# Optimization experiments

Measured on AMD Instinct MI355X. Metric: run time of the kernel, lower is better.

The kernel has to match this reference:

```python
import jax, jax.numpy as jnp
import numpy as np

CUTOFF = 5.0
B, A, N, G, F = 32, 256, 64, 50, 128


def _ssp(v):
    # shifted softplus used by SchNet filter network
    return jax.nn.softplus(v) - jnp.log(2.0).astype(v.dtype)


def setup_inputs() -> dict:
    key = jax.random.key(0)
    ks = jax.random.split(key, 8)
    x = jax.random.normal(ks[0], (B, A, F), dtype=jnp.float32)
    r_ij = jax.random.uniform(ks[1], (B, A, N), dtype=jnp.float32) * 4.5
    f_ij = jax.random.normal(ks[2], (B, A, N, G), dtype=jnp.float32)
    pairwise_mask = jnp.ones((B, A, N), dtype=jnp.float32)
    neighbors = jax.random.randint(ks[3], (B, A, N), 0, A, dtype=jnp.int64)
    in2f_w = jax.random.normal(ks[4], (F, F), dtype=jnp.float32) / np.sqrt(F)
    fw1 = jax.random.normal(ks[5], (G, F), dtype=jnp.float32) / np.sqrt(G)
    fb1 = jnp.zeros((F,), dtype=jnp.float32)
    fw2 = jax.random.normal(ks[6], (F, F), dtype=jnp.float32) / np.sqrt(F)
    fb2 = jnp.zeros((F,), dtype=jnp.float32)
    return {"x": x, "r_ij": r_ij, "f_ij": f_ij, "pairwise_mask": pairwise_mask,
            "neighbors": neighbors, "in2f_w": in2f_w, "fw1": fw1, "fb1": fb1,
            "fw2": fw2, "fb2": fb2}


def reference(x, r_ij, f_ij, pairwise_mask, neighbors, in2f_w, fw1, fb1, fw2, fb2):
    # filter network: Dense(G->F, shifted softplus) -> Dense(F->F, linear)
    W = _ssp(jnp.einsum('bang,gf->banf', f_ij, fw1) + fb1)
    W = jnp.einsum('banh,hf->banf', W, fw2) + fb2          # (B,A,N,F)
    # cosine cutoff
    C = 0.5 * (jnp.cos(r_ij * (jnp.pi / CUTOFF)) + 1.0)
    C = C * (r_ij < CUTOFF).astype(r_ij.dtype)
    W = W * C[..., None]
    # in2f dense (no bias)
    y = jnp.einsum('bai,if->baf', x, in2f_w)               # (B,A,F)
    # gather neighbor features along atom axis
    b_idx = jnp.arange(B)[:, None, None]
    y_nbh = y[b_idx, neighbors]                             # (B,A,N,F)
    # elementwise filter multiply + masked sum over neighbor axis
    out = jnp.sum(y_nbh * W * pairwise_mask[..., None], axis=2)  # (B,A,F)
    return out
```

## Files before the change

kernel.cpp:

```cpp
#include <hip/hip_runtime.h>
#include <hip/hip_bf16.h>
#include <math.h>

#define Bdim 32
#define Adim 256
#define Ndim 64
#define Gdim 50
#define Fdim 128

typedef __attribute__((ext_vector_type(8)))  short short8;
typedef __attribute__((ext_vector_type(16))) float floatx16;

__device__ __forceinline__ unsigned short f2bf_u(float x) {
    __hip_bfloat16 h = __float2bfloat16(x);
    return __builtin_bit_cast(unsigned short, h);
}
__device__ __forceinline__ unsigned pk2bf(float a, float b) {
    return (unsigned)f2bf_u(a) | ((unsigned)f2bf_u(b) << 16);
}
__device__ __forceinline__ float bf2f(unsigned short v) {
    return __builtin_bit_cast(float, ((unsigned)v) << 16);
}
__device__ __forceinline__ float sspf(float v) {
    float t = __expf(-fabsf(v));
    return fmaxf(v, 0.0f) + __logf(1.0f + t) - 0.69314718056f;
}
__device__ __forceinline__ short8 mk8(unsigned a, unsigned b, unsigned c, unsigned d) {
    union { unsigned u[4]; short8 s; } t;
    t.u[0] = a; t.u[1] = b; t.u[2] = c; t.u[3] = d;
    return t.s;
}

__global__ __launch_bounds__(256) void in2f_mfma2(const float* __restrict__ x,
                                                  const float* __restrict__ w,
                                                  unsigned short* __restrict__ y) {
    __shared__ short sWT[128 * 132];
    __shared__ short sX [128 * 132];
    const int tid = threadIdx.x;

#pragma unroll 4
    for (int k = 0; k < 32; ++k) {
        int idx = tid + k * 256;
        float2 v = *(const float2*)(w + 2 * idx);
        int i = idx >> 6;
        int f = (2 * idx) & 127;
        sWT[f * 132 + i]       = (short)f2bf_u(v.x);
        sWT[(f + 1) * 132 + i] = (short)f2bf_u(v.y);
    }
    const float* xb = x + (size_t)blockIdx.x * (128 * 128);
#pragma unroll 4
    for (int k = 0; k < 32; ++k) {
        int idx = tid + k * 256;
        float2 v = *(const float2*)(xb + 2 * idx);
        int row = idx >> 6;
        int i = (2 * idx) & 127;
        *(unsigned*)&sX[row * 132 + i] = pk2bf(v.x, v.y);
    }
    __syncthreads();

    const int wv = tid >> 6, lane = tid & 63, lm = lane & 31, lh = lane >> 5;
    floatx16 acc[4];
#pragma unroll
    for (int jt = 0; jt < 4; ++jt)
#pragma unroll
        for (int e = 0; e < 16; ++e) acc[jt][e] = 0.0f;

#pragma unroll
    for (int ks = 0; ks < 8; ++ks) {
        int g0 = ks * 16 + lh * 8;
        const short* ap = &sX[(wv * 32 + lm) * 132 + g0];
        uint2 a0 = *(const uint2*)ap;
        uint2 a1 = *(const uint2*)(ap + 4);
        short8 a = mk8(a0.x, a0.y, a1.x, a1.y);
#pragma unroll
        for (int jt = 0; jt < 4; ++jt) {
            const short* bp = &sWT[(jt * 32 + lm) * 132 + g0];
            uint2 b0 = *(const uint2*)bp;
            uint2 b1 = *(const uint2*)(bp + 4);
            acc[jt] = __builtin_amdgcn_mfma_f32_32x32x16_bf16(
                a, mk8(b0.x, b0.y, b1.x, b1.y), acc[jt], 0, 0, 0);
        }
    }
    const int rbase = blockIdx.x * 128 + wv * 32;
#pragma unroll
    for (int jt = 0; jt < 4; ++jt)
#pragma unroll
        for (int r = 0; r < 16; ++r) {
            int row = rbase + (r & 3) + 8 * (r >> 2) + 4 * lh;
            y[(size_t)row * 128 + jt * 32 + lm] = f2bf_u(acc[jt][r]);
        }
}

#define SF1 68
#define SF2 132
#define SFI 60

__global__ __launch_bounds__(256, 2) void cfconv_mfma3(
    const float* __restrict__ r_ij, const float* __restrict__ f_ij,
    const float* __restrict__ mask, const int* __restrict__ nbr,
    const float* __restrict__ fw1, const float* __restrict__ fb1,
    const float* __restrict__ fw2, const float* __restrict__ fb2,
    const unsigned short* __restrict__ ybf, float* __restrict__ out)
{
    __shared__ short sFw1[128 * SF1];
    __shared__ short sFw2[128 * SF2];
    __shared__ short sFij[128 * SFI + 16];
    __shared__ float sCm[128];
    __shared__ int   sNbr[128];
    __shared__ float sRed[4 * 128];

    const int tid = threadIdx.x, wv = tid >> 6, lane = tid & 63;
    const int lm = lane & 31, lh = lane >> 5;

    for (int idx = tid; idx < Gdim * 128; idx += 256) {
        int g = idx >> 7, f = idx & 127;
        sFw1[f * SF1 + g] = (short)f2bf_u(fw1[idx]);
    }
    for (int idx = tid; idx < 128 * 14; idx += 256) {
        int f = idx / 14, g = Gdim + idx % 14;
        sFw1[f * SF1 + g] = (g == Gdim) ? (short)f2bf_u(fb1[f]) : (short)0;
    }
    for (int idx = tid; idx < 128 * 128; idx += 256) {
        int h = idx >> 7, f = idx & 127;
        sFw2[f * SF2 + h] = (short)f2bf_u(fw2[idx]);
    }
    for (int idx = tid; idx < 128 * 5; idx += 256) {
        int row = idx / 5, k = idx - row * 5;
        *(unsigned*)&sFij[row * SFI + 50 + 2 * k] = (k == 0) ? 0x00003F80u : 0u;
    }
    if (tid < 8) *(unsigned*)&sFij[128 * SFI + 2 * tid] = 0u;

    float fb2v[4];
#pragma unroll
    for (int jt = 0; jt < 4; ++jt) fb2v[jt] = fb2[jt * 32 + lm];

    for (int it = 0; it < 4; ++it) {
        const int sp = blockIdx.x + 1024 * it;

        const float* fp = f_ij + (size_t)sp * (2 * Ndim * Gdim);
#pragma unroll
        for (int k = 0; k < 13; ++k) {
            int idx = tid + k * 256;
            if (idx < 3200) {
                float2 v = *(const float2*)(fp + 2 * idx);
                int row = idx / 25;
                int g   = 2 * idx - row * 50;
                *(unsigned*)&sFij[row * SFI + g] = pk2bf(v.x, v.y);
            }
        }
        if (tid < 128) {
            int site = sp * 2 + (tid >> 6), n = tid & 63;
            float r = r_ij[(size_t)site * Ndim + n];
            float c = 0.5f * (__cosf(r * 0.62831853071796f) + 1.0f);
            c = (r < 5.0f) ? c : 0.0f;
            sCm[tid]  = c * mask[(size_t)site * Ndim + n];
            sNbr[tid] = nbr[(size_t)site * Ndim + n];
        }
        __syncthreads();

        const int rowb = wv * 32;
        unsigned A2[8][4];
#pragma unroll
        for (int ft = 0; ft < 4; ++ft) {
            floatx16 a1;
#pragma unroll
            for (int e = 0; e < 16; ++e) a1[e] = 0.0f;
#pragma unroll
            for (int ks = 0; ks < 4; ++ks) {
                int g0 = ks * 16 + lh * 8;
                const short* ap = &sFw1[(ft * 32 + lm) * SF1 + g0];
                uint2 a0 = *(const uint2*)ap;
                uint2 a1v = *(const uint2*)(ap + 4);
                const short* bp = &sFij[(rowb + lm) * SFI + g0];
                uint2 b0 = *(const uint2*)bp;
                uint2 b1v = *(const uint2*)(bp + 4);
                a1 = __builtin_amdgcn_mfma_f32_32x32x16_bf16(
                    mk8(a0.x, a0.y, a1v.x, a1v.y),
                    mk8(b0.x, b0.y, b1v.x, b1v.y), a1, 0, 0, 0);
            }
            unsigned P[8], X[8];
#pragma unroll
            for (int q = 0; q < 8; ++q)
                P[q] = pk2bf(sspf(a1[2 * q]), sspf(a1[2 * q + 1]));
#pragma unroll
            for (int q = 0; q < 8; ++q) X[q] = (unsigned)__shfl_xor((int)P[q], 32);
            A2[2*ft][0]   = lh ? X[2] : P[0];  A2[2*ft][1]   = lh ? X[3] : P[1];
            A2[2*ft][2]   = lh ? P[2] : X[0];  A2[2*ft][3]   = lh ? P[3] : X[1];
            A2[2*ft+1][0] = lh ? X[6] : P[4];  A2[2*ft+1][1] = lh ? X[7] : P[5];
            A2[2*ft+1][2] = lh ? P[6] : X[4];  A2[2*ft+1][3] = lh ? P[7] : X[5];
        }

        floatx16 acc2[4];
#pragma unroll
        for (int jt = 0; jt < 4; ++jt)
#pragma unroll
            for (int e = 0; e < 16; ++e) acc2[jt][e] = 0.0f;
#pragma unroll
        for (int ks = 0; ks < 8; ++ks) {
            short8 a = mk8(A2[ks][0], A2[ks][1], A2[ks][2], A2[ks][3]);
#pragma unroll
            for (int jt = 0; jt < 4; ++jt) {
                const short* bp = &sFw2[(jt * 32 + lm) * SF2 + ks * 16 + lh * 8];
                uint2 b0 = *(const uint2*)bp;
                uint2 b1 = *(const uint2*)(bp + 4);
                acc2[jt] = __builtin_amdgcn_mfma_f32_32x32x16_bf16(
                    a, mk8(b0.x, b0.y, b1.x, b1.y), acc2[jt], 0, 0, 0);
            }
        }

        const int ps = sp * 2 + (wv >> 1);
        float cmv[16]; int nbv[16];
#pragma unroll
        for (int rq = 0; rq < 4; ++rq) {
            float4 c4 = *(const float4*)&sCm[wv * 32 + rq * 8 + lh * 4];
            int4   n4 = *(const int4*)&sNbr[wv * 32 + rq * 8 + lh * 4];
            cmv[rq*4+0] = c4.x; cmv[rq*4+1] = c4.y; cmv[rq*4+2] = c4.z; cmv[rq*4+3] = c4.w;
            nbv[rq*4+0] = n4.x; nbv[rq*4+1] = n4.y; nbv[rq*4+2] = n4.z; nbv[rq*4+3] = n4.w;
        }
        const int bofs = (ps >> 8) * Adim;
        float part[4] = {0.f, 0.f, 0.f, 0.f};
#pragma unroll
        for (int r = 0; r < 16; ++r) {
            float cm = cmv[r];
            const unsigned short* yr = ybf + (size_t)(bofs + nbv[r]) * 128;
#pragma unroll
            for (int jt = 0; jt < 4; ++jt) {
                float yv = bf2f(yr[jt * 32 + lm]);
                part[jt] += (acc2[jt][r] + fb2v[jt]) * cm * yv;
            }
        }
#pragma unroll
        for (int jt = 0; jt < 4; ++jt) {
            float s = part[jt] + __shfl_xor(part[jt], 32);
            if (lh == 0) sRed[wv * 128 + jt * 32 + lm] = s;
        }
        __syncthreads();
        {
            int s = tid >> 7, f = tid & 127;
            out[(size_t)(sp * 2 + s) * 128 + f] =
                sRed[(2 * s) * 128 + f] + sRed[(2 * s + 1) * 128 + f];
        }
    }
}

extern "C" void kernel_launch(void* const* d_in, const int* in_sizes, int n_in,
                              void* d_out, int out_size, void* d_ws, size_t ws_size,
                              hipStream_t stream) {
    const float* x      = (const float*)d_in[0];
    const float* r_ij   = (const float*)d_in[1];
    const float* f_ij   = (const float*)d_in[2];
    const float* mask   = (const float*)d_in[3];
    const int*   nbr    = (const int*)d_in[4];
    const float* in2f_w = (const float*)d_in[5];
    const float* fw1    = (const float*)d_in[6];
    const float* fb1    = (const float*)d_in[7];
    const float* fw2    = (const float*)d_in[8];
    const float* fb2    = (const float*)d_in[9];
    float* out = (float*)d_out;
    unsigned short* y = (unsigned short*)d_ws;

    in2f_mfma2<<<64, 256, 0, stream>>>(x, in2f_w, y);
    cfconv_mfma3<<<1024, 256, 0, stream>>>(r_ij, f_ij, mask, nbr,
                                           fw1, fb1, fw2, fb2, y, out);
}
```

Baseline: 253.6 us.

## Move fw1 prep to separate kernel, cut LDS, raise occupancy, cheaper bf16/ssp math

Adds a small prep kernel that writes a transposed bf16 fw1 (with the bias folded in) to workspace, so the main kernel reads it straight from global/L2 and no longer keeps it in shared memory. The freed LDS lets launch bounds go from 2 to 3 blocks per CU. It also swaps the library bf16 conversion for a manual round-to-nearest-even, simplifies the shifted softplus to exp2/log2, hoists the f_ij fragment loads out of the filter loop, and splits in2f over 256 blocks that read x directly from global. Risks: the simplified softplus can overflow for large inputs, the manual rounding does not handle NaN, the extra launch adds overhead, and the higher occupancy target may cause register spills.

```diff
diff --git a/kernel.cpp b/kernel.cpp
--- a/kernel.cpp
+++ b/kernel.cpp
@@ -1,5 +1,4 @@
 #include <hip/hip_runtime.h>
-#include <hip/hip_bf16.h>
 #include <math.h>
 
 #define Bdim 32
@@ -11,19 +10,22 @@
 typedef __attribute__((ext_vector_type(8)))  short short8;
 typedef __attribute__((ext_vector_type(16))) float floatx16;
 
+__device__ __forceinline__ unsigned bfround(float x) {
+    unsigned u = __builtin_bit_cast(unsigned, x);
+    return u + 0x7FFFu + ((u >> 16) & 1u);
+}
 __device__ __forceinline__ unsigned short f2bf_u(float x) {
-    __hip_bfloat16 h = __float2bfloat16(x);
-    return __builtin_bit_cast(unsigned short, h);
+    return (unsigned short)(bfround(x) >> 16);
 }
 __device__ __forceinline__ unsigned pk2bf(float a, float b) {
-    return (unsigned)f2bf_u(a) | ((unsigned)f2bf_u(b) << 16);
+    return (bfround(a) >> 16) | (bfround(b) & 0xFFFF0000u);
 }
 __device__ __forceinline__ float bf2f(unsigned short v) {
     return __builtin_bit_cast(float, ((unsigned)v) << 16);
 }
 __device__ __forceinline__ float sspf(float v) {
-    float t = __expf(-fabsf(v));
-    return fmaxf(v, 0.0f) + __logf(1.0f + t) - 0.69314718056f;
+    float t = __builtin_exp2f(v * 1.44269504089f);
+    return fmaf(__builtin_log2f(1.0f + t), 0.69314718056f, -0.69314718056f);
 }
 __device__ __forceinline__ short8 mk8(unsigned a, unsigned b, unsigned c, unsigned d) {
     union { unsigned u[4]; short8 s; } t;
@@ -31,13 +33,20 @@
     return t.s;
 }
 
-__global__ __launch_bounds__(256) void in2f_mfma2(const float* __restrict__ x,
-                                                  const float* __restrict__ w,
-                                                  unsigned short* __restrict__ y) {
+__global__ __launch_bounds__(256) void prep_fw1t(const float* __restrict__ fw1,
+                                                 const float* __restrict__ fb1,
+                                                 unsigned short* __restrict__ fw1t) {
+    int idx = blockIdx.x * 256 + threadIdx.x;
+    int f = idx >> 6, g = idx & 63;
+    float v = (g < Gdim) ? fw1[g * Fdim + f] : ((g == Gdim) ? fb1[f] : 0.0f);
+    fw1t[idx] = f2bf_u(v);
+}
+
+__global__ __launch_bounds__(256) void in2f_v3(const float* __restrict__ x,
+                                               const float* __restrict__ w,
+                                               unsigned short* __restrict__ y) {
     __shared__ short sWT[128 * 132];
-    __shared__ short sX [128 * 132];
     const int tid = threadIdx.x;
-
 #pragma unroll 4
     for (int k = 0; k < 32; ++k) {
         int idx = tid + k * 256;
@@ -47,62 +56,45 @@
         sWT[f * 132 + i]       = (short)f2bf_u(v.x);
         sWT[(f + 1) * 132 + i] = (short)f2bf_u(v.y);
     }
-    const float* xb = x + (size_t)blockIdx.x * (128 * 128);
-#pragma unroll 4
-    for (int k = 0; k < 32; ++k) {
-        int idx = tid + k * 256;
-        float2 v = *(const float2*)(xb + 2 * idx);
-        int row = idx >> 6;
-        int i = (2 * idx) & 127;
-        *(unsigned*)&sX[row * 132 + i] = pk2bf(v.x, v.y);
-    }
     __syncthreads();
 
     const int wv = tid >> 6, lane = tid & 63, lm = lane & 31, lh = lane >> 5;
-    floatx16 acc[4];
-#pragma unroll
-    for (int jt = 0; jt < 4; ++jt)
-#pragma unroll
-        for (int e = 0; e < 16; ++e) acc[jt][e] = 0.0f;
-
+    const int rbase = blockIdx.x * 32;
+    floatx16 acc;
+#pragma unroll
+    for (int e = 0; e < 16; ++e) acc[e] = 0.0f;
+
+    const float* xr = x + (size_t)(rbase + lm) * Fdim;
 #pragma unroll
     for (int ks = 0; ks < 8; ++ks) {
         int g0 = ks * 16 + lh * 8;
-        const short* ap = &sX[(wv * 32 + lm) * 132 + g0];
-        uint2 a0 = *(const uint2*)ap;
-        uint2 a1 = *(const uint2*)(ap + 4);
-        short8 a = mk8(a0.x, a0.y, a1.x, a1.y);
-#pragma unroll
-        for (int jt = 0; jt < 4; ++jt) {
-            const short* bp = &sWT[(jt * 32 + lm) * 132 + g0];
-            uint2 b0 = *(const uint2*)bp;
-            uint2 b1 = *(const uint2*)(bp + 4);
-            acc[jt] = __builtin_amdgcn_mfma_f32_32x32x16_bf16(
-                a, mk8(b0.x, b0.y, b1.x, b1.y), acc[jt], 0, 0, 0);
-        }
-    }
-    const int rbase = blockIdx.x * 128 + wv * 32;
-#pragma unroll
-    for (int jt = 0; jt < 4; ++jt)
-#pragma unroll
-        for (int r = 0; r < 16; ++r) {
-            int row = rbase + (r & 3) + 8 * (r >> 2) + 4 * lh;
-            y[(size_t)row * 128 + jt * 32 + lm] = f2bf_u(acc[jt][r]);
-        }
-}
-
-#define SF1 68
+        float4 q0 = *(const float4*)(xr + g0);
+        float4 q1 = *(const float4*)(xr + g0 + 4);
+        short8 a = mk8(pk2bf(q0.x, q0.y), pk2bf(q0.z, q0.w),
+                       pk2bf(q1.x, q1.y), pk2bf(q1.z, q1.w));
+        const short* bp = &sWT[(wv * 32 + lm) * 132 + g0];
+        uint2 b0 = *(const uint2*)bp;
+        uint2 b1 = *(const uint2*)(bp + 4);
+        acc = __builtin_amdgcn_mfma_f32_32x32x16_bf16(
+            a, mk8(b0.x, b0.y, b1.x, b1.y), acc, 0, 0, 0);
+    }
+#pragma unroll
+    for (int r = 0; r < 16; ++r) {
+        int row = rbase + (r & 3) + 8 * (r >> 2) + 4 * lh;
+        y[(size_t)row * Fdim + wv * 32 + lm] = f2bf_u(acc[r]);
+    }
+}
+
 #define SF2 132
 #define SFI 60
 
-__global__ __launch_bounds__(256, 2) void cfconv_mfma3(
+__global__ __launch_bounds__(256, 3) void cfconv_v4(
     const float* __restrict__ r_ij, const float* __restrict__ f_ij,
     const float* __restrict__ mask, const int* __restrict__ nbr,
-    const float* __restrict__ fw1, const float* __restrict__ fb1,
+    const unsigned short* __restrict__ fw1t,
     const float* __restrict__ fw2, const float* __restrict__ fb2,
     const unsigned short* __restrict__ ybf, float* __restrict__ out)
 {
-    __shared__ short sFw1[128 * SF1];
     __shared__ short sFw2[128 * SF2];
     __shared__ short sFij[128 * SFI + 16];
     __shared__ float sCm[128];
@@ -112,15 +104,7 @@
     const int tid = threadIdx.x, wv = tid >> 6, lane = tid & 63;
     const int lm = lane & 31, lh = lane >> 5;
 
-    for (int idx = tid; idx < Gdim * 128; idx += 256) {
-        int g = idx >> 7, f = idx & 127;
-        sFw1[f * SF1 + g] = (short)f2bf_u(fw1[idx]);
-    }
-    for (int idx = tid; idx < 128 * 14; idx += 256) {
-        int f = idx / 14, g = Gdim + idx % 14;
-        sFw1[f * SF1 + g] = (g == Gdim) ? (short)f2bf_u(fb1[f]) : (short)0;
-    }
-    for (int idx = tid; idx < 128 * 128; idx += 256) {
+    for (int idx = tid; idx < Fdim * Fdim; idx += 256) {
         int h = idx >> 7, f = idx & 127;
         sFw2[f * SF2 + h] = (short)f2bf_u(fw2[idx]);
     }
@@ -159,6 +143,16 @@
         __syncthreads();
 
         const int rowb = wv * 32;
+        unsigned bfr[4][4];
+#pragma unroll
+        for (int ks = 0; ks < 4; ++ks) {
+            const short* bp = &sFij[(rowb + lm) * SFI + ks * 16 + lh * 8];
+            uint2 b0 = *(const uint2*)bp;
+            uint2 b1 = *(const uint2*)(bp + 4);
+            bfr[ks][0] = b0.x; bfr[ks][1] = b0.y;
+            bfr[ks][2] = b1.x; bfr[ks][3] = b1.y;
+        }
+
         unsigned A2[8][4];
 #pragma unroll
         for (int ft = 0; ft < 4; ++ft) {
@@ -167,16 +161,11 @@
             for (int e = 0; e < 16; ++e) a1[e] = 0.0f;
 #pragma unroll
             for (int ks = 0; ks < 4; ++ks) {
-                int g0 = ks * 16 + lh * 8;
-                const short* ap = &sFw1[(ft * 32 + lm) * SF1 + g0];
-                uint2 a0 = *(const uint2*)ap;
-                uint2 a1v = *(const uint2*)(ap + 4);
-                const short* bp = &sFij[(rowb + lm) * SFI + g0];
-                uint2 b0 = *(const uint2*)bp;
-                uint2 b1v = *(const uint2*)(bp + 4);
+                uint4 av = *(const uint4*)(fw1t + (ft * 32 + lm) * 64 + ks * 16 + lh * 8);
                 a1 = __builtin_amdgcn_mfma_f32_32x32x16_bf16(
-                    mk8(a0.x, a0.y, a1v.x, a1v.y),
-                    mk8(b0.x, b0.y, b1v.x, b1v.y), a1, 0, 0, 0);
+                    mk8(av.x, av.y, av.z, av.w),
+                    mk8(bfr[ks][0], bfr[ks][1], bfr[ks][2], bfr[ks][3]),
+                    a1, 0, 0, 0);
             }
             unsigned P[8], X[8];
 #pragma unroll
@@ -222,7 +211,7 @@
 #pragma unroll
         for (int r = 0; r < 16; ++r) {
             float cm = cmv[r];
-            const unsigned short* yr = ybf + (size_t)(bofs + nbv[r]) * 128;
+            const unsigned short* yr = ybf + (size_t)(bofs + nbv[r]) * Fdim;
 #pragma unroll
             for (int jt = 0; jt < 4; ++jt) {
                 float yv = bf2f(yr[jt * 32 + lm]);
@@ -237,7 +226,7 @@
         __syncthreads();
         {
             int s = tid >> 7, f = tid & 127;
-            out[(size_t)(sp * 2 + s) * 128 + f] =
+            out[(size_t)(sp * 2 + s) * Fdim + f] =
                 sRed[(2 * s) * 128 + f] + sRed[(2 * s + 1) * 128 + f];
         }
     }
@@ -257,9 +246,11 @@
     const float* fw2    = (const float*)d_in[8];
     const float* fb2    = (const float*)d_in[9];
     float* out = (float*)d_out;
-    unsigned short* y = (unsigned short*)d_ws;
-
-    in2f_mfma2<<<64, 256, 0, stream>>>(x, in2f_w, y);
-    cfconv_mfma3<<<1024, 256, 0, stream>>>(r_ij, f_ij, mask, nbr,
-                                           fw1, fb1, fw2, fb2, y, out);
-}
+    unsigned short* y    = (unsigned short*)d_ws;
+    unsigned short* fw1t = y + (size_t)Bdim * Adim * Fdim;
+
+    prep_fw1t<<<32, 256, 0, stream>>>(fw1, fb1, fw1t);
+    in2f_v3<<<256, 256, 0, stream>>>(x, in2f_w, y);
+    cfconv_v4<<<1024, 256, 0, stream>>>(r_ij, f_ij, mask, nbr,
+                                        fw1t, fw2, fb2, y, out);
+}
```

Measured after the change: 345.4 us. 1.36x slower.
